# Optimization experiments

Hardware: AMD Instinct MI355X
Metric: run time of the kernel (lower is better)

## Reference

```python
import jax, jax.numpy as jnp
import numpy as np

NEG_SLOPE = 0.2


def gatv2(x, src, dst, eattr, Wl, bl, Wr, br, We, att, bias, concat):
    # GATv2Conv (PyG semantics): message j->i, softmax over incoming edges of target i.
    n = x.shape[0]
    H, C = att.shape
    xl = (x @ Wl + bl).reshape(n, H, C)   # source transform lin_l
    xr = (x @ Wr + br).reshape(n, H, C)   # target transform lin_r
    xe = (eattr @ We).reshape(-1, H, C)   # edge transform lin_edge (no bias)
    g = jax.nn.leaky_relu(xl[src] + xr[dst] + xe, NEG_SLOPE)  # [E,H,C]
    e = jnp.einsum('ehc,hc->eh', g, att)                      # [E,H]
    m = jax.ops.segment_max(e, dst, num_segments=n)
    a = jnp.exp(e - m[dst])
    s = jax.ops.segment_sum(a, dst, num_segments=n)
    alpha = a / (s[dst] + 1e-16)                              # [E,H]
    out = jax.ops.segment_sum(alpha[:, :, None] * xl[src], dst, num_segments=n)
    out = out.reshape(n, H * C) if concat else out.mean(axis=1)
    return out + bias, alpha


def add_self_loops(src, dst, eattr, n):
    # PyG default: add_self_loops=True, fill_value='mean' for edge_attr
    loop = jnp.arange(n, dtype=src.dtype)
    fill = jnp.broadcast_to(eattr.mean(axis=0, keepdims=True), (n, eattr.shape[1]))
    return (jnp.concatenate([src, loop]), jnp.concatenate([dst, loop]),
            jnp.concatenate([eattr, fill], axis=0))


def setup_inputs() -> dict:
    key = jax.random.key(0)
    ks = iter(jax.random.split(key, 64))
    B, N, D = 4, 2048, 256
    n = B * N
    E = 131072
    H, C1 = 4, 64  # conv1: heads=4, out=hidden//heads=64 (concat -> 256)
    C2 = 256       # conv2: heads=4, out=256, concat=False (mean)
    IN1 = 770

    def rn(shape, s=0.05):
        return jax.random.normal(next(ks), shape, dtype=jnp.float32) * s

    inp = {
        'h': rn((B, N, D), 1.0), 'c_temp': rn((B, N, D), 1.0),
        'c_stereo': rn((B, N, D), 1.0), 'e_proj': rn((B, N, 2), 1.0),
        'f_Lt': rn((B, N, D), 1.0),
        'edges': jax.random.randint(next(ks), (2, E), 0, n, dtype=jnp.int64),
        'edge_attr': rn((E, 1), 1.0),
        # conv1
        'Wl1': rn((IN1, H * C1)), 'bl1': jnp.zeros((H * C1,), jnp.float32),
        'Wr1': rn((IN1, H * C1)), 'br1': jnp.zeros((H * C1,), jnp.float32),
        'We1': rn((1, H * C1)), 'att1': rn((H, C1)),
        'bias1': jnp.zeros((H * C1,), jnp.float32),
        # conv2
        'Wl2': rn((D, H * C2)), 'bl2': jnp.zeros((H * C2,), jnp.float32),
        'Wr2': rn((D, H * C2)), 'br2': jnp.zeros((H * C2,), jnp.float32),
        'We2': rn((1, H * C2)), 'att2': rn((H, C2)),
        'bias2': jnp.zeros((C2,), jnp.float32),
        # GRUCell ([in, 3H] layout; gate order r,z,n as in torch)
        'Wih': rn((D, 3 * D)), 'bih': jnp.zeros((3 * D,), jnp.float32),
        'Whh': rn((D, 3 * D)), 'bhh': jnp.zeros((3 * D,), jnp.float32),
        # heads
        'rW1': rn((D, 256)), 'rb1': jnp.zeros((256,), jnp.float32),
        'rW2': rn((256, 2)), 'rb2': jnp.zeros((2,), jnp.float32),
        'wW1': rn((D, 256)), 'wb1': jnp.zeros((256,), jnp.float32),
        'wW2': rn((256, 2)), 'wb2': jnp.zeros((2,), jnp.float32),
        'pW1': rn((D, 128)), 'pb1': jnp.zeros((128,), jnp.float32),
        'pW2': rn((128, 1)), 'pb2': jnp.zeros((1,), jnp.float32),
        'dW1': rn((D, 128)), 'db1': jnp.zeros((128,), jnp.float32),
        'dW2': rn((128, 1)), 'db2': jnp.zeros((1,), jnp.float32),
    }
    return inp


def reference(h, c_temp, c_stereo, e_proj, f_Lt, edges, edge_attr,
              Wl1, bl1, Wr1, br1, We1, att1, bias1,
              Wl2, bl2, Wr2, br2, We2, att2, bias2,
              Wih, bih, Whh, bhh,
              rW1, rb1, rW2, rb2, wW1, wb1, wW2, wb2,
              pW1, pb1, pW2, pb2, dW1, db1, dW2, db2):
    B, N, D = f_Lt.shape
    n = B * N
    x = jnp.concatenate([c_temp, c_stereo, e_proj, f_Lt], axis=-1).reshape(n, -1)

    src, dst, ea = add_self_loops(edges[0], edges[1], edge_attr, n)
    x1, _ = gatv2(x, src, dst, ea, Wl1, bl1, Wr1, br1, We1, att1, bias1, concat=True)
    x1 = jax.nn.relu(x1)
    x2, alpha = gatv2(x1, src, dst, ea, Wl2, bl2, Wr2, br2, We2, att2, bias2, concat=False)

    # GRUCell
    hf = h.reshape(n, -1)
    gi = x2 @ Wih + bih
    gh = hf @ Whh + bhh
    ir, iz, inew = jnp.split(gi, 3, axis=-1)
    hr, hz, hnew = jnp.split(gh, 3, axis=-1)
    r_g = jax.nn.sigmoid(ir + hr)
    z_g = jax.nn.sigmoid(iz + hz)
    n_g = jnp.tanh(inew + r_g * hnew)
    h_new = ((1.0 - z_g) * n_g + z_g * hf).reshape(B, N, D)

    res = jax.nn.relu(h_new @ rW1 + rb1) @ rW2 + rb2
    w = jax.nn.sigmoid(jax.nn.relu(h_new @ wW1 + wb1) @ wW2 + wb2)
    a_p = jax.nn.softplus(jax.nn.relu(h_new @ pW1 + pb1) @ pW2 + pb2).mean(axis=1)
    a_d = jax.nn.softplus(jax.nn.relu(h_new @ dW1 + db1) @ dW2 + db2)
    return (h_new, res, w, a_p, a_d)
```

## Files before the change

kernel.cpp:

```cpp
#include <hip/hip_runtime.h>
#include <hip/hip_bf16.h>
#include <cstdint>
#include <cstddef>

#define N_NODES 8192
#define E_RAW   131072
#define E_TOT   (E_RAW + N_NODES)
#define HEADS   4

typedef __attribute__((ext_vector_type(8))) __bf16 bf16x8;
typedef __attribute__((ext_vector_type(4))) float f32x4;

__device__ __forceinline__ void gload_lds16(const void* g, void* lds) {
  __builtin_amdgcn_global_load_lds(
      (const __attribute__((address_space(1))) unsigned int*)g,
      (__attribute__((address_space(3))) unsigned int*)lds, 16, 0, 0);
}

__device__ __forceinline__ float bfbits2f(unsigned short u) {
  return __uint_as_float((unsigned)u << 16);
}
__device__ __forceinline__ unsigned short f2bfbits(float f) {
  __hip_bfloat16 b = __float2bfloat16(f);
  return *(unsigned short*)&b;
// ... 137 lines not shown
  __hip_bfloat16* WT = (job < 2) ? WT1 : (job < 4) ? WT2 : (job == 4) ? WTih
                       : (job == 5) ? WThh : WTh;
  __shared__ float sm[32][33];
  int tx = threadIdx.x & 31, ty = threadIdx.x >> 5;
  for (int yy = ty; yy < 32; yy += 8) {
    int k = k0 + yy, n = nb + tx;
    sm[yy][tx] = (k < K && n < N) ? W[(size_t)k * N + n] : 0.f;
  }
  __syncthreads();
  for (int yy = ty; yy < 32; yy += 8) {
    int n = nb + yy, k = k0 + tx;
    if (n < N) WT[(size_t)(n0 + n) * KP + k] = __float2bfloat16(sm[tx][yy]);
  }
}


template <int OUT>
__global__ __launch_bounds__(256) void mfma_gemm(
    const __hip_bfloat16* __restrict__ A, const __hip_bfloat16* __restrict__ BT,
    const float* __restrict__ bias, void* __restrict__ Cout, int KP, int N,
    const __hip_bfloat16* A2, const __hip_bfloat16* BT2,
    const float* bias2, void* C2) {
  if (blockIdx.z == 1) { A = A2; BT = BT2; bias = bias2; Cout = C2; }
  __shared__ uint4 AsBuf[1024];
  __shared__ uint4 BsBuf[1024];
  char* Asc = (char*)AsBuf;
  char* Bsc = (char*)BsBuf;
  int tid = threadIdx.x;
  int lane = tid & 63;
  int wid = tid >> 6;
  int wr = wid >> 1, wc = wid & 1;
  int bm = blockIdx.y * 128;
  int bn = blockIdx.x * 128;
  f32x4 acc[4][4];
#pragma unroll
  for (int i = 0; i < 4; ++i)
#pragma unroll
    for (int j = 0; j < 4; ++j) acc[i][j] = (f32x4){0.f, 0.f, 0.f, 0.f};

  int nK = KP >> 6;
  for (int kt = 0; kt < nK; ++kt) {
    int k0 = kt * 64;
#pragma unroll
    for (int i = 0; i < 4; ++i) {
      int p = i * 256 + tid;
      int row = p >> 3, cc = p & 7;
      int sc = cc ^ (row & 7);
      gload_lds16(A + (size_t)(bm + row) * KP + k0 + sc * 8, Asc + p * 16);
      gload_lds16(BT + (size_t)(bn + row) * KP + k0 + sc * 8, Bsc + p * 16);
    }
    __syncthreads();
#pragma unroll
    for (int s = 0; s < 2; ++s) {
      bf16x8 af[4], bfr[4];
#pragma unroll
      for (int f = 0; f < 4; ++f) {
        int r = wr * 64 + f * 16 + (lane & 15);
        int ch = (s * 4 + (lane >> 4)) ^ (r & 7);
        af[f] = *(const bf16x8*)(Asc + r * 128 + ch * 16);
        int n = wc * 64 + f * 16 + (lane & 15);
        int cb = (s * 4 + (lane >> 4)) ^ (n & 7);
        bfr[f] = *(const bf16x8*)(Bsc + n * 128 + cb * 16);
      }
#pragma unroll
      for (int fm = 0; fm < 4; ++fm)
#pragma unroll
        for (int fn = 0; fn < 4; ++fn)
          acc[fm][fn] = __builtin_amdgcn_mfma_f32_16x16x32_bf16(af[fm], bfr[fn], acc[fm][fn], 0, 0, 0);
    }
    __syncthreads();
  }
  int rbase = bm + wr * 64 + (lane >> 4) * 4;
  int cbase = bn + wc * 64 + (lane & 15);
#pragma unroll
  for (int fm = 0; fm < 4; ++fm)
#pragma unroll
    for (int fn = 0; fn < 4; ++fn) {
      int col = cbase + fn * 16;
      float bv = bias[col];
#pragma unroll
      for (int j = 0; j < 4; ++j) {
        int row = rbase + fm * 16 + j;
        float v = acc[fm][fn][j] + bv;
        if (OUT == 2) v = fmaxf(v, 0.f);
        if (OUT == 0) ((__hip_bfloat16*)Cout)[(size_t)row * N + col] = __float2bfloat16(v);
        else          ((float*)Cout)[(size_t)row * N + col] = v;
      }
    }
}


__global__ __launch_bounds__(256) void gat_fused1(
    const __hip_bfloat16* __restrict__ XLR,
    const int* __restrict__ off, const int* __restrict__ srcn,
    const float* __restrict__ eav, const float* __restrict__ We,
    const float* __restrict__ att, const float* __restrict__ bias,
    __hip_bfloat16* __restrict__ X1) {
  int d = (blockIdx.x * 256 + threadIdx.x) >> 6;
  int lane = threadIdx.x & 63;
  int g = lane >> 4, q = lane & 15;
  int j0 = g * 64 + q * 4;
  const unsigned short* X = (const unsigned short*)XLR;
  ushort4 xrv = *(const ushort4*)(X + (size_t)d * 512 + 256 + j0);
  float xr[4] = {bfbits2f(xrv.x), bfbits2f(xrv.y), bfbits2f(xrv.z), bfbits2f(xrv.w)};
  float4 wev = *(const float4*)(We + j0);
  float4 atv = *(const float4*)(att + j0);
  float we[4] = {wev.x, wev.y, wev.z, wev.w};
  float at[4] = {atv.x, atv.y, atv.z, atv.w};
  int b = off[d], e1 = off[d + 1];
  int pe = e1 - 1;
  int sB = srcn[b]; float eaA = eav[b];
  ushort4 vvA = *(const ushort4*)(X + (size_t)sB * 512 + j0);
  int p1 = (b + 1 <= pe) ? b + 1 : pe;
  sB = srcn[p1]; float eaB = eav[p1];
  float m = -INFINITY, ss = 0.f;
  float a[4] = {0.f, 0.f, 0.f, 0.f};
  for (int p = b; p < e1; ++p) {
    ushort4 vv = vvA; float ea = eaA;
    eaA = eaB;
    vvA = *(const ushort4*)(X + (size_t)sB * 512 + j0);
    int p2 = (p + 2 <= pe) ? p + 2 : pe;
    sB = srcn[p2]; eaB = eav[p2];
    float v[4] = {bfbits2f(vv.x), bfbits2f(vv.y), bfbits2f(vv.z), bfbits2f(vv.w)};
    float t = 0.f;
#pragma unroll
    for (int i = 0; i < 4; ++i) {
      float gg = fmaf(ea, we[i], v[i] + xr[i]);
      float lr = fmaxf(gg, 0.2f * gg);
      t = fmaf(lr, at[i], t);
    }
    t += __shfl_xor(t, 8, 64); t += __shfl_xor(t, 4, 64);
    t += __shfl_xor(t, 2, 64); t += __shfl_xor(t, 1, 64);
    if (__all(t <= m)) {
      float wp = __expf(t - m);
      ss += wp;
#pragma unroll
      for (int i = 0; i < 4; ++i) a[i] = fmaf(wp, v[i], a[i]);
    } else {
      float mn = fmaxf(m, t);
      float scl = __expf(m - mn);
      float wp = __expf(t - mn);
      ss = fmaf(ss, scl, wp);
#pragma unroll
      for (int i = 0; i < 4; ++i) a[i] = fmaf(wp, v[i], a[i] * scl);
      m = mn;
    }
  }
  float inv = 1.f / (ss + 1e-16f);
  unsigned short o[4];
#pragma unroll
  for (int i = 0; i < 4; ++i)
    o[i] = f2bfbits(fmaxf(fmaf(a[i], inv, bias[j0 + i]), 0.f));
  *(ushort4*)((unsigned short*)X1 + (size_t)d * 256 + j0) = *(ushort4*)o;
}


__global__ __launch_bounds__(256) void gat_fused2(
    const __hip_bfloat16* __restrict__ XLR,
    const int* __restrict__ off, const int* __restrict__ srcn,
    const float* __restrict__ eav, const float* __restrict__ We,
    const float* __restrict__ att, const float* __restrict__ bias,
    __hip_bfloat16* __restrict__ X2) {
  int d = (blockIdx.x * 256 + threadIdx.x) >> 6;
  int lane = threadIdx.x & 63;
  int g = lane >> 4, q = lane & 15;
  int j0 = g * 256 + q * 16;
  const unsigned short* X = (const unsigned short*)XLR;
  float xr[16], we[16], at[16];
  {
    const uint4* xp = (const uint4*)(X + (size_t)d * 2048 + 1024 + j0);
    uint4 r0 = xp[0], r1 = xp[1];
    unpk(r0.x, xr[0], xr[1]); unpk(r0.y, xr[2], xr[3]);
    unpk(r0.z, xr[4], xr[5]); unpk(r0.w, xr[6], xr[7]);
    unpk(r1.x, xr[8], xr[9]); unpk(r1.y, xr[10], xr[11]);
    unpk(r1.z, xr[12], xr[13]); unpk(r1.w, xr[14], xr[15]);
#pragma unroll
    for (int i = 0; i < 16; i += 4) {
      float4 w4 = *(const float4*)(We + j0 + i);
      float4 a4 = *(const float4*)(att + j0 + i);
      we[i] = w4.x; we[i + 1] = w4.y; we[i + 2] = w4.z; we[i + 3] = w4.w;
      at[i] = a4.x; at[i + 1] = a4.y; at[i + 2] = a4.z; at[i + 3] = a4.w;
    }
  }
  int b = off[d], e1 = off[d + 1];
  int pe = e1 - 1;
  int sB = srcn[b]; float eaA = eav[b];
  const uint4* rp = (const uint4*)(X + (size_t)sB * 2048 + j0);
  uint4 rA0 = rp[0], rA1 = rp[1];
  int p1 = (b + 1 <= pe) ? b + 1 : pe;
  sB = srcn[p1]; float eaB = eav[p1];
  float m = -INFINITY, ss = 0.f;
  float a[16];
#pragma unroll
  for (int i = 0; i < 16; ++i) a[i] = 0.f;
  for (int p = b; p < e1; ++p) {
    uint4 c0 = rA0, c1 = rA1; float ea = eaA;
    eaA = eaB;
    rp = (const uint4*)(X + (size_t)sB * 2048 + j0);
    rA0 = rp[0]; rA1 = rp[1];
    int p2 = (p + 2 <= pe) ? p + 2 : pe;
    sB = srcn[p2]; eaB = eav[p2];
    float v[16];
    unpk(c0.x, v[0], v[1]); unpk(c0.y, v[2], v[3]);
    unpk(c0.z, v[4], v[5]); unpk(c0.w, v[6], v[7]);
    unpk(c1.x, v[8], v[9]); unpk(c1.y, v[10], v[11]);
    unpk(c1.z, v[12], v[13]); unpk(c1.w, v[14], v[15]);
    float t = 0.f;
#pragma unroll
    for (int i = 0; i < 16; ++i) {
      float gg = fmaf(ea, we[i], v[i] + xr[i]);
      float lr = fmaxf(gg, 0.2f * gg);
      t = fmaf(lr, at[i], t);
    }
    t += __shfl_xor(t, 8, 64); t += __shfl_xor(t, 4, 64);
    t += __shfl_xor(t, 2, 64); t += __shfl_xor(t, 1, 64);
    if (__all(t <= m)) {
      float wp = __expf(t - m);
      ss += wp;
#pragma unroll
      for (int i = 0; i < 16; ++i) a[i] = fmaf(wp, v[i], a[i]);
    } else {
      float mn = fmaxf(m, t);
      float scl = __expf(m - mn);
      float wp = __expf(t - mn);
      ss = fmaf(ss, scl, wp);
#pragma unroll
      for (int i = 0; i < 16; ++i) a[i] = fmaf(wp, v[i], a[i] * scl);
      m = mn;
    }
  }
  float inv = 1.f / (ss + 1e-16f);
#pragma unroll
  for (int i = 0; i < 16; ++i) {
    float r = a[i] * inv;
    r += __shfl_xor(r, 16, 64);
    r += __shfl_xor(r, 32, 64);
    a[i] = r;
  }
  if (g == 0) {
    unsigned short o[16];
#pragma unroll
    for (int i = 0; i < 16; ++i)
      o[i] = f2bfbits(fmaf(0.25f, a[i], bias[q * 16 + i]));
    uint4* op = (uint4*)((unsigned short*)X2 + (size_t)d * 256 + q * 16);
    op[0] = ((uint4*)o)[0];
    op[1] = ((uint4*)o)[1];
  }
}


__global__ void gru_kernel(const float* __restrict__ gi, const float* __restrict__ gh,
                           const float* __restrict__ hf, float* __restrict__ hn,
                           __hip_bfloat16* __restrict__ hnb) {
  int i = blockIdx.x;
  int c = threadIdx.x;
  size_t b = (size_t)i * 768;
  float ir = gi[b + c], iz = gi[b + 256 + c], in_ = gi[b + 512 + c];
  float hr = gh[b + c], hz = gh[b + 256 + c], hn_ = gh[b + 512 + c];
  float r = 1.f / (1.f + __expf(-(ir + hr)));
  float z = 1.f / (1.f + __expf(-(iz + hz)));
  float ng = tanhf(in_ + r * hn_);
  float h0 = hf[(size_t)i * 256 + c];
  float v = (1.f - z) * ng + z * h0;
  hn[(size_t)i * 256 + c] = v;
  hnb[(size_t)i * 256 + c] = __float2bfloat16(v);
}


__global__ __launch_bounds__(256) void heads_final(
    const float* __restrict__ T,
    const float* __restrict__ rW2, const float* __restrict__ rb2,
    const float* __restrict__ wW2, const float* __restrict__ wb2,
    const float* __restrict__ pW2, const float* __restrict__ pb2,
    const float* __restrict__ dW2, const float* __restrict__ db2,
    float* __restrict__ o_res, float* __restrict__ o_w,
    float* __restrict__ AP, float* __restrict__ o_ad) {
  int node = (blockIdx.x * 256 + threadIdx.x) >> 6;
  int lane = threadIdx.x & 63;
  const float* t = T + (size_t)node * 768;
  float4 tr = *(const float4*)(t + lane * 4);
  float4 tw = *(const float4*)(t + 256 + lane * 4);
  float4 tp = {0.f, 0.f, 0.f, 0.f}, td = {0.f, 0.f, 0.f, 0.f};
  if (lane < 32) {
    tp = *(const float4*)(t + 512 + lane * 4);
    td = *(const float4*)(t + 640 + lane * 4);
  }
  float r0 = 0.f, r1 = 0.f, w0 = 0.f, w1 = 0.f, pp = 0.f, dd = 0.f;
#pragma unroll
  for (int i = 0; i < 4; ++i) {
    int k = lane * 4 + i;
    float trv = (i == 0) ? tr.x : (i == 1) ? tr.y : (i == 2) ? tr.z : tr.w;
    float twv = (i == 0) ? tw.x : (i == 1) ? tw.y : (i == 2) ? tw.z : tw.w;
    r0 = fmaf(trv, rW2[k * 2], r0);
    r1 = fmaf(trv, rW2[k * 2 + 1], r1);
    w0 = fmaf(twv, wW2[k * 2], w0);
    w1 = fmaf(twv, wW2[k * 2 + 1], w1);
  }
  if (lane < 32) {
#pragma unroll
    for (int i = 0; i < 4; ++i) {
      int k = lane * 4 + i;
      float tpv = (i == 0) ? tp.x : (i == 1) ? tp.y : (i == 2) ? tp.z : tp.w;
      float tdv = (i == 0) ? td.x : (i == 1) ? td.y : (i == 2) ? td.z : td.w;
      pp = fmaf(tpv, pW2[k], pp);
      dd = fmaf(tdv, dW2[k], dd);
    }
  }
#pragma unroll
  for (int o = 32; o; o >>= 1) {
    r0 += __shfl_xor(r0, o, 64); r1 += __shfl_xor(r1, o, 64);
    w0 += __shfl_xor(w0, o, 64); w1 += __shfl_xor(w1, o, 64);
    pp += __shfl_xor(pp, o, 64); dd += __shfl_xor(dd, o, 64);
  }
  if (lane == 0) {
    o_res[(size_t)node * 2]     = r0 + rb2[0];
    o_res[(size_t)node * 2 + 1] = r1 + rb2[1];
    float sw0 = w0 + wb2[0], sw1 = w1 + wb2[1];
    o_w[(size_t)node * 2]     = 1.f / (1.f + __expf(-sw0));
    o_w[(size_t)node * 2 + 1] = 1.f / (1.f + __expf(-sw1));
    float vp = pp + pb2[0];
    AP[node] = fmaxf(vp, 0.f) + log1pf(__expf(-fabsf(vp)));
    float vd = dd + db2[0];
    o_ad[node] = fmaxf(vd, 0.f) + log1pf(__expf(-fabsf(vd)));
  }
}

__global__ void ap_reduce(const float* __restrict__ ap, float* __restrict__ out) {
  __shared__ float sm[256];
  int b = blockIdx.x, tid = threadIdx.x;
  float acc = 0.f;
  for (int i = tid; i < 2048; i += 256) acc += ap[b * 2048 + i];
  sm[tid] = acc; __syncthreads();
  for (int s = 128; s; s >>= 1) { if (tid < s) sm[tid] += sm[tid + s]; __syncthreads(); }
  if (tid == 0) out[b] = sm[0] * (1.f / 2048.f);
}


extern "C" void kernel_launch(void* const* d_in, const int* in_sizes, int n_in,
                              void* d_out, int out_size, void* d_ws, size_t ws_size,
                              hipStream_t stream) {
  const float* h        = (const float*)d_in[0];
  const float* c_temp   = (const float*)d_in[1];
  const float* c_stereo = (const float*)d_in[2];
  const float* e_proj   = (const float*)d_in[3];
  const float* f_Lt     = (const float*)d_in[4];
  const int*   edges    = (const int*)d_in[5];
  const float* eattr    = (const float*)d_in[6];
  const float* Wl1 = (const float*)d_in[7];  const float* bl1 = (const float*)d_in[8];
  const float* Wr1 = (const float*)d_in[9];  const float* br1 = (const float*)d_in[10];
  const float* We1 = (const float*)d_in[11]; const float* att1 = (const float*)d_in[12];
  const float* bias1 = (const float*)d_in[13];
  const float* Wl2 = (const float*)d_in[14]; const float* bl2 = (const float*)d_in[15];
  const float* Wr2 = (const float*)d_in[16]; const float* br2 = (const float*)d_in[17];
  const float* We2 = (const float*)d_in[18]; const float* att2 = (const float*)d_in[19];
  const float* bias2 = (const float*)d_in[20];
  const float* Wih = (const float*)d_in[21]; const float* bih = (const float*)d_in[22];
  const float* Whh = (const float*)d_in[23]; const float* bhh = (const float*)d_in[24];
  const float* rW1 = (const float*)d_in[25]; const float* rb1 = (const float*)d_in[26];
  const float* rW2 = (const float*)d_in[27]; const float* rb2 = (const float*)d_in[28];
  const float* wW1 = (const float*)d_in[29]; const float* wb1 = (const float*)d_in[30];
  const float* wW2 = (const float*)d_in[31]; const float* wb2 = (const float*)d_in[32];
  const float* pW1 = (const float*)d_in[33]; const float* pb1 = (const float*)d_in[34];
  const float* pW2 = (const float*)d_in[35]; const float* pb2 = (const float*)d_in[36];
  const float* dW1 = (const float*)d_in[37]; const float* db1 = (const float*)d_in[38];
  const float* dW2 = (const float*)d_in[39]; const float* db2 = (const float*)d_in[40];

  const int* src = edges;
  const int* dst = edges + E_RAW;

  float* base = (float*)d_ws;
  size_t cur = 0;
  auto alloc = [&](size_t n) { float* p = base + cur; cur += (n + 63) & ~(size_t)63; return p; };

  float* BIG0 = alloc(8388608);
  float* BIG1 = alloc(6291456);
  float* XLR1f = alloc(2097152);
  float* X1f  = alloc(1048576);
  float* X2f  = alloc(1048576);
  float* Hbf  = alloc(1048576);
  float* HNbf = alloc(1048576);
  float* WT1f = alloc(212992);
  float* WT2f = alloc(262144);
  float* WTihf = alloc(98304);
  float* WThhf = alloc(98304);
  float* WThf  = alloc(98304);
  float* B1 = alloc(512);
  float* B2 = alloc(2048);
  float* BH = alloc(768);
  float* EAV = alloc(E_TOT);
  float* AP  = alloc(N_NODES);
  float* MP  = alloc(320);
  int* ICNT = (int*)alloc(2 * N_NODES);
  int* IOFF = (int*)alloc(N_NODES + 64);
  int* ISRC = (int*)alloc(E_TOT);
  if (ws_size < cur * 4) return;
  int* IPOS = ICNT + N_NODES;

  __hip_bfloat16* x_bf = (__hip_bfloat16*)BIG1;
  __hip_bfloat16* XLR1 = (__hip_bfloat16*)XLR1f;
  __hip_bfloat16* XLR2 = (__hip_bfloat16*)BIG0;
  __hip_bfloat16* X1b = (__hip_bfloat16*)X1f;
  __hip_bfloat16* X2b = (__hip_bfloat16*)X2f;
  __hip_bfloat16* Hb  = (__hip_bfloat16*)Hbf;
  __hip_bfloat16* HNb = (__hip_bfloat16*)HNbf;
  __hip_bfloat16* WT1 = (__hip_bfloat16*)WT1f;
  __hip_bfloat16* WT2 = (__hip_bfloat16*)WT2f;
  __hip_bfloat16* WTih = (__hip_bfloat16*)WTihf;
  __hip_bfloat16* WThh = (__hip_bfloat16*)WThhf;
  __hip_bfloat16* WTh  = (__hip_bfloat16*)WThf;
  float* gi = BIG0;
  float* gh = BIG1;
  float* T  = BIG0;

  float* o_hnew = (float*)d_out;
  float* o_res  = o_hnew + (size_t)N_NODES * 256;
  float* o_w    = o_res + (size_t)N_NODES * 2;
  float* o_ap   = o_w + (size_t)N_NODES * 2;
  float* o_ad   = o_ap + 4;

  prep_kernel<<<9549, 256, 0, stream>>>(c_temp, c_stereo, e_proj, f_Lt, h, eattr,
                                        bl1, br1, bl2, br2, rb1, wb1, pb1, db1,
                                        x_bf, Hb, MP, ICNT, B1, B2, BH);
  csr_count<<<(E_TOT + 255) / 256, 256, 0, stream>>>(dst, ICNT);
  csr_scan<<<1, 1024, 0, stream>>>(ICNT, IOFF, MP);
  csr_fill<<<(E_TOT + 255) / 256, 256, 0, stream>>>(src, dst, eattr, MP + 256,
                                                    IOFF, IPOS, ISRC, EAV);
  wt_all<<<1504, 256, 0, stream>>>(Wl1, Wr1, Wl2, Wr2, Wih, Whh, rW1, wW1, pW1, dW1,
                                   WT1, WT2, WTih, WThh, WTh);

  mfma_gemm<0><<<dim3(4, 64, 1), 256, 0, stream>>>(x_bf, WT1, B1, XLR1, 832, 512,
                                                   nullptr, nullptr, nullptr, nullptr);
  gat_fused1<<<N_NODES / 4, 256, 0, stream>>>(XLR1, IOFF, ISRC, EAV, We1, att1, bias1, X1b);

  mfma_gemm<0><<<dim3(16, 64, 1), 256, 0, stream>>>(X1b, WT2, B2, XLR2, 256, 2048,
                                                    nullptr, nullptr, nullptr, nullptr);
  gat_fused2<<<N_NODES / 4, 256, 0, stream>>>(XLR2, IOFF, ISRC, EAV, We2, att2, bias2, X2b);

  mfma_gemm<1><<<dim3(6, 64, 2), 256, 0, stream>>>(X2b, WTih, bih, gi, 256, 768,
                                                   Hb, WThh, bhh, gh);
  gru_kernel<<<N_NODES, 256, 0, stream>>>(gi, gh, h, o_hnew, HNb);

  mfma_gemm<2><<<dim3(6, 64, 1), 256, 0, stream>>>(HNb, WTh, BH, T, 256, 768,
                                                   nullptr, nullptr, nullptr, nullptr);
  heads_final<<<N_NODES / 4, 256, 0, stream>>>(T, rW2, rb2, wW2, wb2, pW2, pb2, dW2, db2,
                                               o_res, o_w, AP, o_ad);
  ap_reduce<<<4, 256, 0, stream>>>(AP, o_ap);
}
```

Measured before the change: 216.4 us.

## Split GAT edge loops across four waves per node and store GEMM intermediates in bf16

```diff
diff --git a/kernel.cpp b/kernel.cpp
--- a/kernel.cpp
+++ b/kernel.cpp
@@ -243,22 +243,27 @@
       for (int j = 0; j < 4; ++j) {
         int row = rbase + fm * 16 + j;
         float v = acc[fm][fn][j] + bv;
-        if (OUT == 2) v = fmaxf(v, 0.f);
-        if (OUT == 0) ((__hip_bfloat16*)Cout)[(size_t)row * N + col] = __float2bfloat16(v);
-        else          ((float*)Cout)[(size_t)row * N + col] = v;
+        if (OUT == 2 || OUT == 3) v = fmaxf(v, 0.f);
+        if (OUT == 0 || OUT == 3)
+          ((__hip_bfloat16*)Cout)[(size_t)row * N + col] = __float2bfloat16(v);
+        else
+          ((float*)Cout)[(size_t)row * N + col] = v;
       }
     }
 }
 
 
-__global__ __launch_bounds__(256) void gat_fused1(
+__global__ __launch_bounds__(256, 4) void gat_fused1(
     const __hip_bfloat16* __restrict__ XLR,
     const int* __restrict__ off, const int* __restrict__ srcn,
     const float* __restrict__ eav, const float* __restrict__ We,
     const float* __restrict__ att, const float* __restrict__ bias,
     __hip_bfloat16* __restrict__ X1) {
-  int d = (blockIdx.x * 256 + threadIdx.x) >> 6;
-  int lane = threadIdx.x & 63;
+  __shared__ float lds_a[4][256];
+  __shared__ float sm_m[4][4], sm_ss[4][4], sst[4];
+  int d = blockIdx.x;
+  int tid = threadIdx.x;
+  int w = tid >> 6, lane = tid & 63;
   int g = lane >> 4, q = lane & 15;
   int j0 = g * 64 + q * 4;
   const unsigned short* X = (const unsigned short*)XLR;
@@ -268,62 +273,80 @@
   float4 atv = *(const float4*)(att + j0);
   float we[4] = {wev.x, wev.y, wev.z, wev.w};
   float at[4] = {atv.x, atv.y, atv.z, atv.w};
-  int b = off[d], e1 = off[d + 1];
-  int pe = e1 - 1;
-  int sB = srcn[b]; float eaA = eav[b];
-  ushort4 vvA = *(const ushort4*)(X + (size_t)sB * 512 + j0);
-  int p1 = (b + 1 <= pe) ? b + 1 : pe;
-  sB = srcn[p1]; float eaB = eav[p1];
+  int b = off[d], deg = off[d + 1] - b;
+  int nw = (deg > w) ? ((deg - w + 3) >> 2) : 0;
   float m = -INFINITY, ss = 0.f;
   float a[4] = {0.f, 0.f, 0.f, 0.f};
-  for (int p = b; p < e1; ++p) {
-    ushort4 vv = vvA; float ea = eaA;
-    eaA = eaB;
-    vvA = *(const ushort4*)(X + (size_t)sB * 512 + j0);
-    int p2 = (p + 2 <= pe) ? p + 2 : pe;
-    sB = srcn[p2]; eaB = eav[p2];
-    float v[4] = {bfbits2f(vv.x), bfbits2f(vv.y), bfbits2f(vv.z), bfbits2f(vv.w)};
-    float t = 0.f;
-#pragma unroll
-    for (int i = 0; i < 4; ++i) {
-      float gg = fmaf(ea, we[i], v[i] + xr[i]);
-      float lr = fmaxf(gg, 0.2f * gg);
-      t = fmaf(lr, at[i], t);
-    }
-    t += __shfl_xor(t, 8, 64); t += __shfl_xor(t, 4, 64);
-    t += __shfl_xor(t, 2, 64); t += __shfl_xor(t, 1, 64);
-    if (__all(t <= m)) {
-      float wp = __expf(t - m);
-      ss += wp;
-#pragma unroll
-      for (int i = 0; i < 4; ++i) a[i] = fmaf(wp, v[i], a[i]);
-    } else {
-      float mn = fmaxf(m, t);
-      float scl = __expf(m - mn);
-      float wp = __expf(t - mn);
-      ss = fmaf(ss, scl, wp);
-#pragma unroll
-      for (int i = 0; i < 4; ++i) a[i] = fmaf(wp, v[i], a[i] * scl);
-      m = mn;
-    }
-  }
-  float inv = 1.f / (ss + 1e-16f);
-  unsigned short o[4];
-#pragma unroll
-  for (int i = 0; i < 4; ++i)
-    o[i] = f2bfbits(fmaxf(fmaf(a[i], inv, bias[j0 + i]), 0.f));
-  *(ushort4*)((unsigned short*)X1 + (size_t)d * 256 + j0) = *(ushort4*)o;
-}
-
-
-__global__ __launch_bounds__(256) void gat_fused2(
+  if (nw > 0) {
+    int p0 = b + w;
+    int pe = p0 + 4 * (nw - 1);
+    int sB = srcn[p0]; float eaA = eav[p0];
+    ushort4 vvA = *(const ushort4*)(X + (size_t)sB * 512 + j0);
+    int p1 = min(p0 + 4, pe);
+    sB = srcn[p1]; float eaB = eav[p1];
+    for (int k = 0; k < nw; ++k) {
+      ushort4 vv = vvA; float ea = eaA;
+      eaA = eaB;
+      vvA = *(const ushort4*)(X + (size_t)sB * 512 + j0);
+      int p2 = min(p0 + 4 * (k + 2), pe);
+      sB = srcn[p2]; eaB = eav[p2];
+      float v[4] = {bfbits2f(vv.x), bfbits2f(vv.y), bfbits2f(vv.z), bfbits2f(vv.w)};
+      float t = 0.f;
+#pragma unroll
+      for (int i = 0; i < 4; ++i) {
+        float gg = fmaf(ea, we[i], v[i] + xr[i]);
+        float lr = fmaxf(gg, 0.2f * gg);
+        t = fmaf(lr, at[i], t);
+      }
+      t += __shfl_xor(t, 8, 64); t += __shfl_xor(t, 4, 64);
+      t += __shfl_xor(t, 2, 64); t += __shfl_xor(t, 1, 64);
+      if (__all(t <= m)) {
+        float wp = __expf(t - m);
+        ss += wp;
+#pragma unroll
+        for (int i = 0; i < 4; ++i) a[i] = fmaf(wp, v[i], a[i]);
+      } else {
+        float mn = fmaxf(m, t);
+        float scl = __expf(m - mn);
+        float wp = __expf(t - mn);
+        ss = fmaf(ss, scl, wp);
+#pragma unroll
+        for (int i = 0; i < 4; ++i) a[i] = fmaf(wp, v[i], a[i] * scl);
+        m = mn;
+      }
+    }
+  }
+  if (q == 0) { sm_m[w][g] = m; sm_ss[w][g] = ss; }
+  __syncthreads();
+  float M = fmaxf(fmaxf(sm_m[0][g], sm_m[1][g]), fmaxf(sm_m[2][g], sm_m[3][g]));
+  float scale = __expf(m - M);
+#pragma unroll
+  for (int i = 0; i < 4; ++i) lds_a[w][j0 + i] = a[i] * scale;
+  if (w == 0 && q == 0) {
+    float st = 1e-16f;
+#pragma unroll
+    for (int ww = 0; ww < 4; ++ww) st += sm_ss[ww][g] * __expf(sm_m[ww][g] - M);
+    sst[g] = st;
+  }
+  __syncthreads();
+  int c = tid;
+  float val = lds_a[0][c] + lds_a[1][c] + lds_a[2][c] + lds_a[3][c];
+  float outv = val / sst[c >> 6] + bias[c];
+  X1[(size_t)d * 256 + c] = __float2bfloat16(fmaxf(outv, 0.f));
+}
+
+
+__global__ __launch_bounds__(256, 4) void gat_fused2(
     const __hip_bfloat16* __restrict__ XLR,
     const int* __restrict__ off, const int* __restrict__ srcn,
     const float* __restrict__ eav, const float* __restrict__ We,
     const float* __restrict__ att, const float* __restrict__ bias,
     __hip_bfloat16* __restrict__ X2) {
-  int d = (blockIdx.x * 256 + threadIdx.x) >> 6;
-  int lane = threadIdx.x & 63;
+  __shared__ float lds_a[4][1024];
+  __shared__ float sm_m[4][4], sm_ss[4][4], sst[4];
+  int d = blockIdx.x;
+  int tid = threadIdx.x;
+  int w = tid >> 6, lane = tid & 63;
   int g = lane >> 4, q = lane & 15;
   int j0 = g * 256 + q * 16;
   const unsigned short* X = (const unsigned short*)XLR;
@@ -343,81 +366,96 @@
       at[i] = a4.x; at[i + 1] = a4.y; at[i + 2] = a4.z; at[i + 3] = a4.w;
     }
   }
-  int b = off[d], e1 = off[d + 1];
-  int pe = e1 - 1;
-  int sB = srcn[b]; float eaA = eav[b];
-  const uint4* rp = (const uint4*)(X + (size_t)sB * 2048 + j0);
-  uint4 rA0 = rp[0], rA1 = rp[1];
-  int p1 = (b + 1 <= pe) ? b + 1 : pe;
-  sB = srcn[p1]; float eaB = eav[p1];
+  int b = off[d], deg = off[d + 1] - b;
+  int nw = (deg > w) ? ((deg - w + 3) >> 2) : 0;
   float m = -INFINITY, ss = 0.f;
   float a[16];
 #pragma unroll
   for (int i = 0; i < 16; ++i) a[i] = 0.f;
-  for (int p = b; p < e1; ++p) {
-    uint4 c0 = rA0, c1 = rA1; float ea = eaA;
-    eaA = eaB;
-    rp = (const uint4*)(X + (size_t)sB * 2048 + j0);
-    rA0 = rp[0]; rA1 = rp[1];
-    int p2 = (p + 2 <= pe) ? p + 2 : pe;
-    sB = srcn[p2]; eaB = eav[p2];
-    float v[16];
-    unpk(c0.x, v[0], v[1]); unpk(c0.y, v[2], v[3]);
-    unpk(c0.z, v[4], v[5]); unpk(c0.w, v[6], v[7]);
-    unpk(c1.x, v[8], v[9]); unpk(c1.y, v[10], v[11]);
-    unpk(c1.z, v[12], v[13]); unpk(c1.w, v[14], v[15]);
-    float t = 0.f;
-#pragma unroll
-    for (int i = 0; i < 16; ++i) {
-      float gg = fmaf(ea, we[i], v[i] + xr[i]);
-      float lr = fmaxf(gg, 0.2f * gg);
-      t = fmaf(lr, at[i], t);
-    }
-    t += __shfl_xor(t, 8, 64); t += __shfl_xor(t, 4, 64);
-    t += __shfl_xor(t, 2, 64); t += __shfl_xor(t, 1, 64);
-    if (__all(t <= m)) {
-      float wp = __expf(t - m);
-      ss += wp;
-#pragma unroll
-      for (int i = 0; i < 16; ++i) a[i] = fmaf(wp, v[i], a[i]);
-    } else {
-      float mn = fmaxf(m, t);
-      float scl = __expf(m - mn);
-      float wp = __expf(t - mn);
-      ss = fmaf(ss, scl, wp);
-#pragma unroll
-      for (int i = 0; i < 16; ++i) a[i] = fmaf(wp, v[i], a[i] * scl);
-      m = mn;
-    }
-  }
-  float inv = 1.f / (ss + 1e-16f);
+  if (nw > 0) {
+    int p0 = b + w;
+    int pe = p0 + 4 * (nw - 1);
+    int sB = srcn[p0]; float eaA = eav[p0];
+    const uint4* rp = (const uint4*)(X + (size_t)sB * 2048 + j0);
+    uint4 rA0 = rp[0], rA1 = rp[1];
+    int p1 = min(p0 + 4, pe);
+    sB = srcn[p1]; float eaB = eav[p1];
+    for (int k = 0; k < nw; ++k) {
+      uint4 c0 = rA0, c1 = rA1; float ea = eaA;
+      eaA = eaB;
+      rp = (const uint4*)(X + (size_t)sB * 2048 + j0);
+      rA0 = rp[0]; rA1 = rp[1];
+      int p2 = min(p0 + 4 * (k + 2), pe);
+      sB = srcn[p2]; eaB = eav[p2];
+      float v[16];
+      unpk(c0.x, v[0], v[1]); unpk(c0.y, v[2], v[3]);
+      unpk(c0.z, v[4], v[5]); unpk(c0.w, v[6], v[7]);
+      unpk(c1.x, v[8], v[9]); unpk(c1.y, v[10], v[11]);
+      unpk(c1.z, v[12], v[13]); unpk(c1.w, v[14], v[15]);
+      float t = 0.f;
+#pragma unroll
+      for (int i = 0; i < 16; ++i) {
+        float gg = fmaf(ea, we[i], v[i] + xr[i]);
+        float lr = fmaxf(gg, 0.2f * gg);
+        t = fmaf(lr, at[i], t);
+      }
+      t += __shfl_xor(t, 8, 64); t += __shfl_xor(t, 4, 64);
+      t += __shfl_xor(t, 2, 64); t += __shfl_xor(t, 1, 64);
+      if (__all(t <= m)) {
+        float wp = __expf(t - m);
+        ss += wp;
+#pragma unroll
+        for (int i = 0; i < 16; ++i) a[i] = fmaf(wp, v[i], a[i]);
+      } else {
+        float mn = fmaxf(m, t);
+        float scl = __expf(m - mn);
+        float wp = __expf(t - mn);
+        ss = fmaf(ss, scl, wp);
+#pragma unroll
+        for (int i = 0; i < 16; ++i) a[i] = fmaf(wp, v[i], a[i] * scl);
+        m = mn;
+      }
+    }
+  }
+  if (q == 0) { sm_m[w][g] = m; sm_ss[w][g] = ss; }
+  __syncthreads();
+  float M = fmaxf(fmaxf(sm_m[0][g], sm_m[1][g]), fmaxf(sm_m[2][g], sm_m[3][g]));
+  float scale = __expf(m - M);
 #pragma unroll
   for (int i = 0; i < 16; ++i) {
-    float r = a[i] * inv;
-    r += __shfl_xor(r, 16, 64);
-    r += __shfl_xor(r, 32, 64);
-    a[i] = r;
-  }
-  if (g == 0) {
-    unsigned short o[16];
-#pragma unroll
-    for (int i = 0; i < 16; ++i)
-      o[i] = f2bfbits(fmaf(0.25f, a[i], bias[q * 16 + i]));
-    uint4* op = (uint4*)((unsigned short*)X2 + (size_t)d * 256 + q * 16);
-    op[0] = ((uint4*)o)[0];
-    op[1] = ((uint4*)o)[1];
-  }
-}
-
-
-__global__ void gru_kernel(const float* __restrict__ gi, const float* __restrict__ gh,
+    int ir = (i + q) & 15;
+    lds_a[w][j0 + ir] = a[ir] * scale;
+  }
+  if (w == 0 && q == 0) {
+    float st = 1e-16f;
+#pragma unroll
+    for (int ww = 0; ww < 4; ++ww) st += sm_ss[ww][g] * __expf(sm_m[ww][g] - M);
+    sst[g] = st;
+  }
+  __syncthreads();
+  int c = tid;
+  float acc = 0.f;
+#pragma unroll
+  for (int hh = 0; hh < 4; ++hh) {
+    int addr = hh * 256 + c;
+    float sv = lds_a[0][addr] + lds_a[1][addr] + lds_a[2][addr] + lds_a[3][addr];
+    acc += sv / sst[hh];
+  }
+  X2[(size_t)d * 256 + c] = __float2bfloat16(fmaf(0.25f, acc, bias[c]));
+}
+
+
+__global__ void gru_kernel(const __hip_bfloat16* __restrict__ gi,
+                           const __hip_bfloat16* __restrict__ gh,
                            const float* __restrict__ hf, float* __restrict__ hn,
                            __hip_bfloat16* __restrict__ hnb) {
   int i = blockIdx.x;
   int c = threadIdx.x;
   size_t b = (size_t)i * 768;
-  float ir = gi[b + c], iz = gi[b + 256 + c], in_ = gi[b + 512 + c];
-  float hr = gh[b + c], hz = gh[b + 256 + c], hn_ = gh[b + 512 + c];
+  const unsigned short* giu = (const unsigned short*)gi;
+  const unsigned short* ghu = (const unsigned short*)gh;
+  float ir = bfbits2f(giu[b + c]), iz = bfbits2f(giu[b + 256 + c]), in_ = bfbits2f(giu[b + 512 + c]);
+  float hr = bfbits2f(ghu[b + c]), hz = bfbits2f(ghu[b + 256 + c]), hn_ = bfbits2f(ghu[b + 512 + c]);
   float r = 1.f / (1.f + __expf(-(ir + hr)));
   float z = 1.f / (1.f + __expf(-(iz + hz)));
   float ng = tanhf(in_ + r * hn_);
@@ -429,7 +467,7 @@
 
 
 __global__ __launch_bounds__(256) void heads_final(
-    const float* __restrict__ T,
+    const __hip_bfloat16* __restrict__ Tb,
     const float* __restrict__ rW2, const float* __restrict__ rb2,
     const float* __restrict__ wW2, const float* __restrict__ wb2,
     const float* __restrict__ pW2, const float* __restrict__ pb2,
@@ -438,33 +476,33 @@
     float* __restrict__ AP, float* __restrict__ o_ad) {
   int node = (blockIdx.x * 256 + threadIdx.x) >> 6;
   int lane = threadIdx.x & 63;
-  const float* t = T + (size_t)node * 768;
-  float4 tr = *(const float4*)(t + lane * 4);
-  float4 tw = *(const float4*)(t + 256 + lane * 4);
-  float4 tp = {0.f, 0.f, 0.f, 0.f}, td = {0.f, 0.f, 0.f, 0.f};
+  const unsigned short* t = (const unsigned short*)Tb + (size_t)node * 768;
+  ushort4 tr = *(const ushort4*)(t + lane * 4);
+  ushort4 tw = *(const ushort4*)(t + 256 + lane * 4);
+  float trf[4] = {bfbits2f(tr.x), bfbits2f(tr.y), bfbits2f(tr.z), bfbits2f(tr.w)};
+  float twf[4] = {bfbits2f(tw.x), bfbits2f(tw.y), bfbits2f(tw.z), bfbits2f(tw.w)};
+  float tpf[4] = {0.f, 0.f, 0.f, 0.f}, tdf[4] = {0.f, 0.f, 0.f, 0.f};
   if (lane < 32) {
-    tp = *(const float4*)(t + 512 + lane * 4);
-    td = *(const float4*)(t + 640 + lane * 4);
+    ushort4 tp = *(const ushort4*)(t + 512 + lane * 4);
+    ushort4 td = *(const ushort4*)(t + 640 + lane * 4);
+    tpf[0] = bfbits2f(tp.x); tpf[1] = bfbits2f(tp.y); tpf[2] = bfbits2f(tp.z); tpf[3] = bfbits2f(tp.w);
+    tdf[0] = bfbits2f(td.x); tdf[1] = bfbits2f(td.y); tdf[2] = bfbits2f(td.z); tdf[3] = bfbits2f(td.w);
   }
   float r0 = 0.f, r1 = 0.f, w0 = 0.f, w1 = 0.f, pp = 0.f, dd = 0.f;
 #pragma unroll
   for (int i = 0; i < 4; ++i) {
     int k = lane * 4 + i;
-    float trv = (i == 0) ? tr.x : (i == 1) ? tr.y : (i == 2) ? tr.z : tr.w;
-    float twv = (i == 0) ? tw.x : (i == 1) ? tw.y : (i == 2) ? tw.z : tw.w;
-    r0 = fmaf(trv, rW2[k * 2], r0);
-    r1 = fmaf(trv, rW2[k * 2 + 1], r1);
-    w0 = fmaf(twv, wW2[k * 2], w0);
-    w1 = fmaf(twv, wW2[k * 2 + 1], w1);
+    r0 = fmaf(trf[i], rW2[k * 2], r0);
+    r1 = fmaf(trf[i], rW2[k * 2 + 1], r1);
+    w0 = fmaf(twf[i], wW2[k * 2], w0);
+    w1 = fmaf(twf[i], wW2[k * 2 + 1], w1);
   }
   if (lane < 32) {
 #pragma unroll
     for (int i = 0; i < 4; ++i) {
       int k = lane * 4 + i;
-      float tpv = (i == 0) ? tp.x : (i == 1) ? tp.y : (i == 2) ? tp.z : tp.w;
-      float tdv = (i == 0) ? td.x : (i == 1) ? td.y : (i == 2) ? td.z : td.w;
-      pp = fmaf(tpv, pW2[k], pp);
-      dd = fmaf(tdv, dW2[k], dd);
+      pp = fmaf(tpf[i], pW2[k], pp);
+      dd = fmaf(tdf[i], dW2[k], dd);
     }
   }
 #pragma unroll
@@ -569,9 +607,9 @@
   __hip_bfloat16* WTih = (__hip_bfloat16*)WTihf;
   __hip_bfloat16* WThh = (__hip_bfloat16*)WThhf;
   __hip_bfloat16* WTh  = (__hip_bfloat16*)WThf;
-  float* gi = BIG0;
-  float* gh = BIG1;
-  float* T  = BIG0;
+  __hip_bfloat16* gi = (__hip_bfloat16*)BIG0;
+  __hip_bfloat16* gh = (__hip_bfloat16*)BIG1;
+  __hip_bfloat16* Tb = (__hip_bfloat16*)BIG0;
 
   float* o_hnew = (float*)d_out;
   float* o_res  = o_hnew + (size_t)N_NODES * 256;
@@ -591,19 +629,19 @@
 
   mfma_gemm<0><<<dim3(4, 64, 1), 256, 0, stream>>>(x_bf, WT1, B1, XLR1, 832, 512,
                                                    nullptr, nullptr, nullptr, nullptr);
-  gat_fused1<<<N_NODES / 4, 256, 0, stream>>>(XLR1, IOFF, ISRC, EAV, We1, att1, bias1, X1b);
+  gat_fused1<<<N_NODES, 256, 0, stream>>>(XLR1, IOFF, ISRC, EAV, We1, att1, bias1, X1b);
 
   mfma_gemm<0><<<dim3(16, 64, 1), 256, 0, stream>>>(X1b, WT2, B2, XLR2, 256, 2048,
                                                     nullptr, nullptr, nullptr, nullptr);
-  gat_fused2<<<N_NODES / 4, 256, 0, stream>>>(XLR2, IOFF, ISRC, EAV, We2, att2, bias2, X2b);
-
-  mfma_gemm<1><<<dim3(6, 64, 2), 256, 0, stream>>>(X2b, WTih, bih, gi, 256, 768,
+  gat_fused2<<<N_NODES, 256, 0, stream>>>(XLR2, IOFF, ISRC, EAV, We2, att2, bias2, X2b);
+
+  mfma_gemm<0><<<dim3(6, 64, 2), 256, 0, stream>>>(X2b, WTih, bih, gi, 256, 768,
                                                    Hb, WThh, bhh, gh);
   gru_kernel<<<N_NODES, 256, 0, stream>>>(gi, gh, h, o_hnew, HNb);
 
-  mfma_gemm<2><<<dim3(6, 64, 1), 256, 0, stream>>>(HNb, WTh, BH, T, 256, 768,
+  mfma_gemm<3><<<dim3(6, 64, 1), 256, 0, stream>>>(HNb, WTh, BH, Tb, 256, 768,
                                                    nullptr, nullptr, nullptr, nullptr);
-  heads_final<<<N_NODES / 4, 256, 0, stream>>>(T, rW2, rb2, wW2, wb2, pW2, pb2, dW2, db2,
+  heads_final<<<N_NODES / 4, 256, 0, stream>>>(Tb, rW2, rb2, wW2, wb2, pW2, pb2, dW2, db2,
                                                o_res, o_w, AP, o_ad);
   ap_reduce<<<4, 256, 0, stream>>>(AP, o_ap);
 }
```

New measurement: 229.0 us. 1.06x slower.

## Deepen gather prefetch in GAT kernels and store GEMM intermediates in bf16

Applied to the files above, without the earlier changes.

```diff
diff --git a/kernel.cpp b/kernel.cpp
--- a/kernel.cpp
+++ b/kernel.cpp
@@ -243,15 +243,17 @@
       for (int j = 0; j < 4; ++j) {
         int row = rbase + fm * 16 + j;
         float v = acc[fm][fn][j] + bv;
-        if (OUT == 2) v = fmaxf(v, 0.f);
-        if (OUT == 0) ((__hip_bfloat16*)Cout)[(size_t)row * N + col] = __float2bfloat16(v);
-        else          ((float*)Cout)[(size_t)row * N + col] = v;
+        if (OUT == 2 || OUT == 3) v = fmaxf(v, 0.f);
+        if (OUT == 0 || OUT == 3)
+          ((__hip_bfloat16*)Cout)[(size_t)row * N + col] = __float2bfloat16(v);
+        else
+          ((float*)Cout)[(size_t)row * N + col] = v;
       }
     }
 }
 
 
-__global__ __launch_bounds__(256) void gat_fused1(
+__global__ __launch_bounds__(256, 4) void gat_fused1(
     const __hip_bfloat16* __restrict__ XLR,
     const int* __restrict__ off, const int* __restrict__ srcn,
     const float* __restrict__ eav, const float* __restrict__ We,
@@ -259,8 +261,8 @@
     __hip_bfloat16* __restrict__ X1) {
   int d = (blockIdx.x * 256 + threadIdx.x) >> 6;
   int lane = threadIdx.x & 63;
-  int g = lane >> 4, q = lane & 15;
-  int j0 = g * 64 + q * 4;
+  int q = lane & 15;
+  int j0 = (lane >> 4) * 64 + q * 4;
   const unsigned short* X = (const unsigned short*)XLR;
   ushort4 xrv = *(const ushort4*)(X + (size_t)d * 512 + 256 + j0);
   float xr[4] = {bfbits2f(xrv.x), bfbits2f(xrv.y), bfbits2f(xrv.z), bfbits2f(xrv.w)};
@@ -269,19 +271,26 @@
   float we[4] = {wev.x, wev.y, wev.z, wev.w};
   float at[4] = {atv.x, atv.y, atv.z, atv.w};
   int b = off[d], e1 = off[d + 1];
+  int deg = e1 - b;
   int pe = e1 - 1;
-  int sB = srcn[b]; float eaA = eav[b];
-  ushort4 vvA = *(const ushort4*)(X + (size_t)sB * 512 + j0);
-  int p1 = (b + 1 <= pe) ? b + 1 : pe;
-  sB = srcn[p1]; float eaB = eav[p1];
+  int nch = (deg + 3) >> 2;
   float m = -INFINITY, ss = 0.f;
   float a[4] = {0.f, 0.f, 0.f, 0.f};
-  for (int p = b; p < e1; ++p) {
-    ushort4 vv = vvA; float ea = eaA;
-    eaA = eaB;
-    vvA = *(const ushort4*)(X + (size_t)sB * 512 + j0);
-    int p2 = (p + 2 <= pe) ? p + 2 : pe;
-    sB = srcn[p2]; eaB = eav[p2];
+
+  auto ldidx = [&](int c, int4& s4, float4& e4) {
+    int base = b + 4 * c;
+    int p0 = min(base, pe), p1 = min(base + 1, pe);
+    int p2 = min(base + 2, pe), p3 = min(base + 3, pe);
+    s4.x = srcn[p0]; s4.y = srcn[p1]; s4.z = srcn[p2]; s4.w = srcn[p3];
+    e4.x = eav[p0];  e4.y = eav[p1];  e4.z = eav[p2];  e4.w = eav[p3];
+  };
+  auto ldrows = [&](const int4& s4, ushort4* R) {
+    R[0] = *(const ushort4*)(X + (size_t)s4.x * 512 + j0);
+    R[1] = *(const ushort4*)(X + (size_t)s4.y * 512 + j0);
+    R[2] = *(const ushort4*)(X + (size_t)s4.z * 512 + j0);
+    R[3] = *(const ushort4*)(X + (size_t)s4.w * 512 + j0);
+  };
+  auto proc = [&](ushort4 vv, float ea, bool valid) {
     float v[4] = {bfbits2f(vv.x), bfbits2f(vv.y), bfbits2f(vv.z), bfbits2f(vv.w)};
     float t = 0.f;
 #pragma unroll
@@ -292,6 +301,7 @@
     }
     t += __shfl_xor(t, 8, 64); t += __shfl_xor(t, 4, 64);
     t += __shfl_xor(t, 2, 64); t += __shfl_xor(t, 1, 64);
+    if (!valid) t = -1e30f;
     if (__all(t <= m)) {
       float wp = __expf(t - m);
       ss += wp;
@@ -306,17 +316,42 @@
       for (int i = 0; i < 4; ++i) a[i] = fmaf(wp, v[i], a[i] * scl);
       m = mn;
     }
+  };
+
+  int4 sA, sB; float4 eA, eB, eT;
+  ushort4 RA[4], RB[4];
+  ldidx(0, sA, eA);
+  ldrows(sA, RA);
+  ldidx(1, sB, eB);
+  for (int c = 0; c < nch; c += 2) {
+    ldrows(sB, RB);
+    ldidx(c + 2, sA, eT);
+    int base = b + 4 * c;
+    proc(RA[0], eA.x, base < e1);
+    proc(RA[1], eA.y, base + 1 < e1);
+    proc(RA[2], eA.z, base + 2 < e1);
+    proc(RA[3], eA.w, base + 3 < e1);
+    float4 eBc = eB;
+    ldrows(sA, RA);
+    ldidx(c + 3, sB, eB);
+    eA = eT;
+    proc(RB[0], eBc.x, base + 4 < e1);
+    proc(RB[1], eBc.y, base + 5 < e1);
+    proc(RB[2], eBc.z, base + 6 < e1);
+    proc(RB[3], eBc.w, base + 7 < e1);
   }
   float inv = 1.f / (ss + 1e-16f);
+  float4 bv = *(const float4*)(bias + j0);
+  float bb[4] = {bv.x, bv.y, bv.z, bv.w};
   unsigned short o[4];
 #pragma unroll
   for (int i = 0; i < 4; ++i)
-    o[i] = f2bfbits(fmaxf(fmaf(a[i], inv, bias[j0 + i]), 0.f));
+    o[i] = f2bfbits(fmaxf(fmaf(a[i], inv, bb[i]), 0.f));
   *(ushort4*)((unsigned short*)X1 + (size_t)d * 256 + j0) = *(ushort4*)o;
 }
 
 
-__global__ __launch_bounds__(256) void gat_fused2(
+__global__ __launch_bounds__(256, 2) void gat_fused2(
     const __hip_bfloat16* __restrict__ XLR,
     const int* __restrict__ off, const int* __restrict__ srcn,
     const float* __restrict__ eav, const float* __restrict__ We,
@@ -344,23 +379,32 @@
     }
   }
   int b = off[d], e1 = off[d + 1];
+  int deg = e1 - b;
   int pe = e1 - 1;
-  int sB = srcn[b]; float eaA = eav[b];
-  const uint4* rp = (const uint4*)(X + (size_t)sB * 2048 + j0);
-  uint4 rA0 = rp[0], rA1 = rp[1];
-  int p1 = (b + 1 <= pe) ? b + 1 : pe;
-  sB = srcn[p1]; float eaB = eav[p1];
+  int nch = (deg + 3) >> 2;
   float m = -INFINITY, ss = 0.f;
   float a[16];
 #pragma unroll
   for (int i = 0; i < 16; ++i) a[i] = 0.f;
-  for (int p = b; p < e1; ++p) {
-    uint4 c0 = rA0, c1 = rA1; float ea = eaA;
-    eaA = eaB;
-    rp = (const uint4*)(X + (size_t)sB * 2048 + j0);
-    rA0 = rp[0]; rA1 = rp[1];
-    int p2 = (p + 2 <= pe) ? p + 2 : pe;
-    sB = srcn[p2]; eaB = eav[p2];
+
+  auto ldidx = [&](int c, int4& s4, float4& e4) {
+    int base = b + 4 * c;
+    int p0 = min(base, pe), p1 = min(base + 1, pe);
+    int p2 = min(base + 2, pe), p3 = min(base + 3, pe);
+    s4.x = srcn[p0]; s4.y = srcn[p1]; s4.z = srcn[p2]; s4.w = srcn[p3];
+    e4.x = eav[p0];  e4.y = eav[p1];  e4.z = eav[p2];  e4.w = eav[p3];
+  };
+  auto ldrows = [&](const int4& s4, uint4* R) {
+    const uint4* p0 = (const uint4*)(X + (size_t)s4.x * 2048 + j0);
+    const uint4* p1 = (const uint4*)(X + (size_t)s4.y * 2048 + j0);
+    const uint4* p2 = (const uint4*)(X + (size_t)s4.z * 2048 + j0);
+    const uint4* p3 = (const uint4*)(X + (size_t)s4.w * 2048 + j0);
+    R[0] = p0[0]; R[1] = p0[1];
+    R[2] = p1[0]; R[3] = p1[1];
+    R[4] = p2[0]; R[5] = p2[1];
+    R[6] = p3[0]; R[7] = p3[1];
+  };
+  auto proc = [&](uint4 c0, uint4 c1, float ea, bool valid) {
     float v[16];
     unpk(c0.x, v[0], v[1]); unpk(c0.y, v[2], v[3]);
     unpk(c0.z, v[4], v[5]); unpk(c0.w, v[6], v[7]);
@@ -375,6 +419,7 @@
     }
     t += __shfl_xor(t, 8, 64); t += __shfl_xor(t, 4, 64);
     t += __shfl_xor(t, 2, 64); t += __shfl_xor(t, 1, 64);
+    if (!valid) t = -1e30f;
     if (__all(t <= m)) {
       float wp = __expf(t - m);
       ss += wp;
@@ -389,6 +434,29 @@
       for (int i = 0; i < 16; ++i) a[i] = fmaf(wp, v[i], a[i] * scl);
       m = mn;
     }
+  };
+
+  int4 sA, sB; float4 eA, eB, eT;
+  uint4 RA[8], RB[8];
+  ldidx(0, sA, eA);
+  ldrows(sA, RA);
+  ldidx(1, sB, eB);
+  for (int c = 0; c < nch; c += 2) {
+    ldrows(sB, RB);
+    ldidx(c + 2, sA, eT);
+    int base = b + 4 * c;
+    proc(RA[0], RA[1], eA.x, base < e1);
+    proc(RA[2], RA[3], eA.y, base + 1 < e1);
+    proc(RA[4], RA[5], eA.z, base + 2 < e1);
+    proc(RA[6], RA[7], eA.w, base + 3 < e1);
+    float4 eBc = eB;
+    ldrows(sA, RA);
+    ldidx(c + 3, sB, eB);
+    eA = eT;
+    proc(RB[0], RB[1], eBc.x, base + 4 < e1);
+    proc(RB[2], RB[3], eBc.y, base + 5 < e1);
+    proc(RB[4], RB[5], eBc.z, base + 6 < e1);
+    proc(RB[6], RB[7], eBc.w, base + 7 < e1);
   }
   float inv = 1.f / (ss + 1e-16f);
 #pragma unroll
@@ -410,14 +478,17 @@
 }
 
 
-__global__ void gru_kernel(const float* __restrict__ gi, const float* __restrict__ gh,
+__global__ void gru_kernel(const __hip_bfloat16* __restrict__ gi,
+                           const __hip_bfloat16* __restrict__ gh,
                            const float* __restrict__ hf, float* __restrict__ hn,
                            __hip_bfloat16* __restrict__ hnb) {
   int i = blockIdx.x;
   int c = threadIdx.x;
   size_t b = (size_t)i * 768;
-  float ir = gi[b + c], iz = gi[b + 256 + c], in_ = gi[b + 512 + c];
-  float hr = gh[b + c], hz = gh[b + 256 + c], hn_ = gh[b + 512 + c];
+  const unsigned short* giu = (const unsigned short*)gi;
+  const unsigned short* ghu = (const unsigned short*)gh;
+  float ir = bfbits2f(giu[b + c]), iz = bfbits2f(giu[b + 256 + c]), in_ = bfbits2f(giu[b + 512 + c]);
+  float hr = bfbits2f(ghu[b + c]), hz = bfbits2f(ghu[b + 256 + c]), hn_ = bfbits2f(ghu[b + 512 + c]);
   float r = 1.f / (1.f + __expf(-(ir + hr)));
   float z = 1.f / (1.f + __expf(-(iz + hz)));
   float ng = tanhf(in_ + r * hn_);
@@ -429,7 +500,7 @@
 
 
 __global__ __launch_bounds__(256) void heads_final(
-    const float* __restrict__ T,
+    const __hip_bfloat16* __restrict__ Tb,
     const float* __restrict__ rW2, const float* __restrict__ rb2,
     const float* __restrict__ wW2, const float* __restrict__ wb2,
     const float* __restrict__ pW2, const float* __restrict__ pb2,
@@ -438,33 +509,33 @@
     float* __restrict__ AP, float* __restrict__ o_ad) {
   int node = (blockIdx.x * 256 + threadIdx.x) >> 6;
   int lane = threadIdx.x & 63;
-  const float* t = T + (size_t)node * 768;
-  float4 tr = *(const float4*)(t + lane * 4);
-  float4 tw = *(const float4*)(t + 256 + lane * 4);
-  float4 tp = {0.f, 0.f, 0.f, 0.f}, td = {0.f, 0.f, 0.f, 0.f};
+  const unsigned short* t = (const unsigned short*)Tb + (size_t)node * 768;
+  ushort4 tr = *(const ushort4*)(t + lane * 4);
+  ushort4 tw = *(const ushort4*)(t + 256 + lane * 4);
+  float trf[4] = {bfbits2f(tr.x), bfbits2f(tr.y), bfbits2f(tr.z), bfbits2f(tr.w)};
+  float twf[4] = {bfbits2f(tw.x), bfbits2f(tw.y), bfbits2f(tw.z), bfbits2f(tw.w)};
+  float tpf[4] = {0.f, 0.f, 0.f, 0.f}, tdf[4] = {0.f, 0.f, 0.f, 0.f};
   if (lane < 32) {
-    tp = *(const float4*)(t + 512 + lane * 4);
-    td = *(const float4*)(t + 640 + lane * 4);
+    ushort4 tp = *(const ushort4*)(t + 512 + lane * 4);
+    ushort4 td = *(const ushort4*)(t + 640 + lane * 4);
+    tpf[0] = bfbits2f(tp.x); tpf[1] = bfbits2f(tp.y); tpf[2] = bfbits2f(tp.z); tpf[3] = bfbits2f(tp.w);
+    tdf[0] = bfbits2f(td.x); tdf[1] = bfbits2f(td.y); tdf[2] = bfbits2f(td.z); tdf[3] = bfbits2f(td.w);
   }
   float r0 = 0.f, r1 = 0.f, w0 = 0.f, w1 = 0.f, pp = 0.f, dd = 0.f;
 #pragma unroll
   for (int i = 0; i < 4; ++i) {
     int k = lane * 4 + i;
-    float trv = (i == 0) ? tr.x : (i == 1) ? tr.y : (i == 2) ? tr.z : tr.w;
-    float twv = (i == 0) ? tw.x : (i == 1) ? tw.y : (i == 2) ? tw.z : tw.w;
-    r0 = fmaf(trv, rW2[k * 2], r0);
-    r1 = fmaf(trv, rW2[k * 2 + 1], r1);
-    w0 = fmaf(twv, wW2[k * 2], w0);
-    w1 = fmaf(twv, wW2[k * 2 + 1], w1);
+    r0 = fmaf(trf[i], rW2[k * 2], r0);
+    r1 = fmaf(trf[i], rW2[k * 2 + 1], r1);
+    w0 = fmaf(twf[i], wW2[k * 2], w0);
+    w1 = fmaf(twf[i], wW2[k * 2 + 1], w1);
   }
   if (lane < 32) {
 #pragma unroll
     for (int i = 0; i < 4; ++i) {
       int k = lane * 4 + i;
-      float tpv = (i == 0) ? tp.x : (i == 1) ? tp.y : (i == 2) ? tp.z : tp.w;
-      float tdv = (i == 0) ? td.x : (i == 1) ? td.y : (i == 2) ? td.z : td.w;
-      pp = fmaf(tpv, pW2[k], pp);
-      dd = fmaf(tdv, dW2[k], dd);
+      pp = fmaf(tpf[i], pW2[k], pp);
+      dd = fmaf(tdf[i], dW2[k], dd);
     }
   }
 #pragma unroll
@@ -569,9 +640,9 @@
   __hip_bfloat16* WTih = (__hip_bfloat16*)WTihf;
   __hip_bfloat16* WThh = (__hip_bfloat16*)WThhf;
   __hip_bfloat16* WTh  = (__hip_bfloat16*)WThf;
-  float* gi = BIG0;
-  float* gh = BIG1;
-  float* T  = BIG0;
+  __hip_bfloat16* gi = (__hip_bfloat16*)BIG0;
+  __hip_bfloat16* gh = (__hip_bfloat16*)BIG1;
+  __hip_bfloat16* Tb = (__hip_bfloat16*)BIG0;
 
   float* o_hnew = (float*)d_out;
   float* o_res  = o_hnew + (size_t)N_NODES * 256;
@@ -597,13 +668,13 @@
                                                     nullptr, nullptr, nullptr, nullptr);
   gat_fused2<<<N_NODES / 4, 256, 0, stream>>>(XLR2, IOFF, ISRC, EAV, We2, att2, bias2, X2b);
 
-  mfma_gemm<1><<<dim3(6, 64, 2), 256, 0, stream>>>(X2b, WTih, bih, gi, 256, 768,
+  mfma_gemm<0><<<dim3(6, 64, 2), 256, 0, stream>>>(X2b, WTih, bih, gi, 256, 768,
                                                    Hb, WThh, bhh, gh);
   gru_kernel<<<N_NODES, 256, 0, stream>>>(gi, gh, h, o_hnew, HNb);
 
-  mfma_gemm<2><<<dim3(6, 64, 1), 256, 0, stream>>>(HNb, WTh, BH, T, 256, 768,
+  mfma_gemm<3><<<dim3(6, 64, 1), 256, 0, stream>>>(HNb, WTh, BH, Tb, 256, 768,
                                                    nullptr, nullptr, nullptr, nullptr);
-  heads_final<<<N_NODES / 4, 256, 0, stream>>>(T, rW2, rb2, wW2, wb2, pW2, pb2, dW2, db2,
+  heads_final<<<N_NODES / 4, 256, 0, stream>>>(Tb, rW2, rb2, wW2, wb2, pW2, pb2, dW2, db2,
                                                o_res, o_w, AP, o_ad);
   ap_reduce<<<4, 256, 0, stream>>>(AP, o_ap);
 }
```

Result: slower. 230.4 us (+6.5%).
